# Optimization experiments

Hardware: AMD Instinct MI355X
Metric: run time of the kernel (lower is better)

## Reference

```python
import jax, jax.numpy as jnp
import numpy as np

B, H, S, D = 4, 16, 2048, 128


def setup_inputs() -> dict:
    key = jax.random.key(0)
    kq, kk, kv, km = jax.random.split(key, 4)
    query = jax.random.normal(kq, (B, H, S, D), dtype=jnp.float32)
    k = jax.random.normal(kk, (B, H, S, D), dtype=jnp.float32)
    value = jax.random.normal(kv, (B, H, S, D), dtype=jnp.float32)
    mask = jax.random.randint(km, (B, 1, S, S), 0, 2, dtype=jnp.int32)
    return {"query": query, "key": k, "value": value, "mask": mask, "softmax_dim": -1}


def reference(query, key, value, mask, softmax_dim):
    dk = query.shape[-1]
    # scores: [B, H, S, S]
    scores = jnp.einsum("bhqd,bhkd->bhqk", query, key) / jnp.sqrt(jnp.float32(dk))
    scores = jnp.where(mask == 0, jnp.float32(-1e9), scores)
    attention = jax.nn.softmax(scores, axis=softmax_dim)
    out = jnp.einsum("bhqk,bhkd->bhqd", attention, value)
    return (out, attention)
```

## Files before the change

kernel.cpp:

```cpp
#include <hip/hip_runtime.h>

typedef __attribute__((ext_vector_type(8))) short short8;
typedef __attribute__((ext_vector_type(4))) short short4v;
typedef __attribute__((ext_vector_type(4))) float float4v;

#define B_ 4
#define H_ 16
#define S_ 2048
#define D_ 128
#define BM 64
#define NKT64 32
#define NKT32 64

#define NSH (B_ * H_ * S_ * D_)
#define NMW ((size_t)B_ * 32 * S_)
#define WS_NEED (3ull * (unsigned long long)NSH * 2ull + (unsigned long long)NMW * 8ull)

#define QSCALE (0.08838834764831845f * 1.4426950408889634f)

__device__ __forceinline__ short f2bf(float f) {
  unsigned u = __float_as_uint(f);
  u = (u + 0x7fffu + ((u >> 16) & 1u)) >> 16;
  return (short)u;
}

__device__ __forceinline__ void gl16(const void* g, void* lds) {
  __builtin_amdgcn_global_load_lds(
      (const __attribute__((address_space(1))) unsigned int*)g,
      (__attribute__((address_space(3))) unsigned int*)lds, 16, 0, 0);
}

__global__ void prep_q(const float* __restrict__ Qg, short* __restrict__ Qb) {
  size_t id = (size_t)blockIdx.x * 256 + threadIdx.x;
  const float4v* src = (const float4v*)(Qg + id * 8);
  float4v a = src[0], b = src[1];
  short8 s;
  s[0] = f2bf(a[0] * QSCALE); s[1] = f2bf(a[1] * QSCALE);
  s[2] = f2bf(a[2] * QSCALE); s[3] = f2bf(a[3] * QSCALE);
  s[4] = f2bf(b[0] * QSCALE); s[5] = f2bf(b[1] * QSCALE);
  s[6] = f2bf(b[2] * QSCALE); s[7] = f2bf(b[3] * QSCALE);
  *((short8*)Qb + id) = s;
}

__global__ void prep_k(const float* __restrict__ Kg, short* __restrict__ Kf) {
  size_t id = (size_t)blockIdx.x * 256 + threadIdx.x;
  int c  = (int)(id & 15);
  int g  = (int)((id >> 4) & 3);
  int dc = (int)((id >> 6) & 3);
  int kf = (int)((id >> 8) & 3);
  int kt = (int)((id >> 10) & 31);
  size_t bh = id >> 15;
  const float* src = Kg + ((bh * S_ + (size_t)(kt * 64 + kf * 16 + c)) * D_) + dc * 32 + g * 8;
  float4v a = *(const float4v*)src;
  float4v b = *(const float4v*)(src + 4);
  short8 s;
  s[0] = f2bf(a[0]); s[1] = f2bf(a[1]); s[2] = f2bf(a[2]); s[3] = f2bf(a[3]);
  s[4] = f2bf(b[0]); s[5] = f2bf(b[1]); s[6] = f2bf(b[2]); s[7] = f2bf(b[3]);
  *((short8*)Kf + id) = s;
}

__global__ void prep_v(const float* __restrict__ Vg, short* __restrict__ Vf) {
  size_t id = (size_t)blockIdx.x * 256 + threadIdx.x;
  int c   = (int)(id & 15);
  int g   = (int)((id >> 4) & 3);
  int df  = (int)((id >> 6) & 7);
  int kt32= (int)((id >> 9) & 63);
  size_t bh = id >> 15;
  const float* src = Vg + (bh * S_ + (size_t)(kt32 * 32 + g * 8)) * D_ + df * 16 + c;
  short8 s;
#pragma unroll
  for (int e = 0; e < 8; ++e) s[e] = f2bf(src[(size_t)e * D_]);
  *((short8*)Vf + id) = s;
}

__global__ void prep_m(const int* __restrict__ Mg, unsigned long long* __restrict__ Bits) {
  int gw = blockIdx.x * 4 + (threadIdx.x >> 6);
  int j  = threadIdx.x & 63;
  int kt = gw & 31;
  int q  = (gw >> 5) & (S_ - 1);
  int b  = gw >> 16;
  int m = Mg[((size_t)b * S_ + q) * S_ + kt * 64 + j];
  unsigned long long bal = __ballot(m != 0);
  if (j == 0) Bits[((size_t)b * 32 + kt) * S_ + q] = bal;
}

__global__ __launch_bounds__(256, 4) void sdpa_main(
    const short* __restrict__ Qb, const short* __restrict__ Kfr,
    const short* __restrict__ Vfr, const unsigned long long* __restrict__ Bits,
    float* __restrict__ Og, float* __restrict__ Ag) {

  __shared__ __align__(16) char smem[32768 + 5120];
  short (*Ps)[40] = (short (*)[40])(smem + 32768);

  const int t = threadIdx.x;
  const int w = t >> 6;
  const int l = t & 63;
  const int g = l >> 4;
  const int c = l & 15;

  const int bid = blockIdx.x;
  const int qt = bid & 31;
  const int h  = (bid >> 5) & 15;
  const int b  = bid >> 9;

  const int qbase  = qt * BM;
  const int qrow_l = w * 16 + c;
  const int qrow   = qbase + qrow_l;

  const size_t bhOff = (size_t)(b * H_ + h) * (S_ * D_);
  const short* Qp  = Qb  + bhOff;
  const short* Kp  = Kfr + bhOff;
  const short* Vp  = Vfr + bhOff;
  const unsigned long long* Bp = Bits + (size_t)b * 32 * S_;
  const unsigned* Bu = (const unsigned*)Bits;
  float* Op = Og + bhOff;
  float* Ap = Ag + (size_t)(b * H_ + h) * ((size_t)S_ * S_);

  short8 qf[4];
#pragma unroll
  for (int dc = 0; dc < 4; ++dc)
    qf[dc] = *(const short8*)(Qp + (size_t)qrow * D_ + dc * 32 + g * 8);

#pragma unroll
  for (int i = 0; i < 4; ++i) {
    int f = w * 4 + i;
    gl16(Kp + f * 512 + l * 8, smem + f * 1024);
  }
  __syncthreads();

  float ls0 = 0.f, ls1 = 0.f, ls2 = 0.f, ls3 = 0.f;
  int cur = 0;
  for (int kt = 0; kt < NKT64; ++kt) {
    if (kt < NKT64 - 1) {
      const short* src = Kp + (size_t)(kt + 1) * 8192;
      char* dst = smem + (cur ^ 1) * 16384;
#pragma unroll
      for (int i = 0; i < 4; ++i) {
        int f = w * 4 + i;
        gl16(src + f * 512 + l * 8, dst + f * 1024);
      }
    }
    unsigned long long mb = Bp[(size_t)kt * S_ + qrow];
    const char* kb = smem + cur * 16384;

    float4v acc[4];
#pragma unroll
    for (int kf = 0; kf < 4; ++kf) acc[kf] = (float4v){0.f, 0.f, 0.f, 0.f};
#pragma unroll
    for (int kf = 0; kf < 4; ++kf) {
#pragma unroll
      for (int dc = 0; dc < 4; ++dc) {
        short8 af = *(const short8*)(kb + (kf * 4 + dc) * 1024 + l * 16);
        acc[kf] = __builtin_amdgcn_mfma_f32_16x16x32_bf16(af, qf[dc], acc[kf], 0, 0, 0);
      }
    }
#pragma unroll
    for (int kf = 0; kf < 4; ++kf) {
      unsigned mg = (unsigned)(mb >> (kf * 16 + g * 4)) & 0xFu;
      float p0 = ((mg >> 0) & 1) ? __builtin_amdgcn_exp2f(acc[kf][0]) : 0.f;
      float p1 = ((mg >> 1) & 1) ? __builtin_amdgcn_exp2f(acc[kf][1]) : 0.f;
      float p2 = ((mg >> 2) & 1) ? __builtin_amdgcn_exp2f(acc[kf][2]) : 0.f;
      float p3 = ((mg >> 3) & 1) ? __builtin_amdgcn_exp2f(acc[kf][3]) : 0.f;
      if (kf == 0) ls0 += (p0 + p1) + (p2 + p3);
      else if (kf == 1) ls1 += (p0 + p1) + (p2 + p3);
      else if (kf == 2) ls2 += (p0 + p1) + (p2 + p3);
      else ls3 += (p0 + p1) + (p2 + p3);
    }
    __syncthreads();
    cur ^= 1;
  }
  float lsum = (ls0 + ls1) + (ls2 + ls3);
  lsum += __shfl_xor(lsum, 16);
  lsum += __shfl_xor(lsum, 32);
  const float rl = (lsum > 0.f) ? (1.0f / lsum) : 0.f;

#pragma unroll
  for (int i = 0; i < 2; ++i) {
    int f = w + 4 * i;
    gl16(Kp + f * 512 + l * 8, smem + f * 1024);
    gl16(Vp + f * 512 + l * 8, smem + 16384 + f * 1024);
  }
  __syncthreads();

  float4v acco[8];
#pragma unroll
  for (int df = 0; df < 8; ++df) acco[df] = (float4v){0.f, 0.f, 0.f, 0.f};

  cur = 0;
  for (int kt = 0; kt < NKT32; ++kt) {
    if (kt < NKT32 - 1) {
      const short* ks = Kp + (size_t)(kt + 1) * 4096;
      const short* vs = Vp + (size_t)(kt + 1) * 4096;
      char* kd = smem + (cur ^ 1) * 8192;
      char* vd = smem + 16384 + (cur ^ 1) * 8192;
#pragma unroll
      for (int i = 0; i < 2; ++i) {
        int f = w + 4 * i;
        gl16(ks + f * 512 + l * 8, kd + f * 1024);
        gl16(vs + f * 512 + l * 8, vd + f * 1024);
      }
    }
    unsigned mw = Bu[((size_t)(b * 32 + (kt >> 1)) * S_ + qrow) * 2 + (kt & 1)];
    const char* kb = smem + cur * 8192;
    const char* vb = smem + 16384 + cur * 8192;

    float4v acc[2];
#pragma unroll
    for (int kf = 0; kf < 2; ++kf) acc[kf] = (float4v){0.f, 0.f, 0.f, 0.f};
#pragma unroll
    for (int kf = 0; kf < 2; ++kf) {
#pragma unroll
      for (int dc = 0; dc < 4; ++dc) {
        short8 af = *(const short8*)(kb + (kf * 4 + dc) * 1024 + l * 16);
        acc[kf] = __builtin_amdgcn_mfma_f32_16x16x32_bf16(af, qf[dc], acc[kf], 0, 0, 0);
      }
    }

#pragma unroll
    for (int kf = 0; kf < 2; ++kf) {
      int k0 = kt * 32 + kf * 16 + g * 4;
      unsigned mg = (mw >> (kf * 16 + g * 4)) & 0xFu;
      float4v aw;
      short4v pb;
#pragma unroll
      for (int r = 0; r < 4; ++r) {
        float pn = ((mg >> r) & 1) ? __builtin_amdgcn_exp2f(acc[kf][r]) * rl : 0.f;
        aw[r] = pn;
        pb[r] = f2bf(pn);
      }
      __builtin_nontemporal_store(aw, (float4v*)(Ap + (size_t)qrow * S_ + k0));
      *(short4v*)&Ps[qrow_l][kf * 16 + g * 4] = pb;
    }

    {
      short8 pbf = *(const short8*)&Ps[qrow_l][g * 8];
#pragma unroll
      for (int df = 0; df < 8; ++df) {
        short8 vf = *(const short8*)(vb + df * 1024 + l * 16);
        acco[df] = __builtin_amdgcn_mfma_f32_16x16x32_bf16(vf, pbf, acco[df], 0, 0, 0);
      }
    }
    __syncthreads();
    cur ^= 1;
  }

#pragma unroll
  for (int df = 0; df < 8; ++df) {
    *(float4v*)(Op + (size_t)qrow * D_ + df * 16 + g * 4) = acco[df];
  }
}

#define LQK 136
#define LVT 72

__global__ __launch_bounds__(256, 3) void sdpa_fallback(
    const float* __restrict__ Qg, const float* __restrict__ Kg,
    const float* __restrict__ Vg, const int* __restrict__ Mg,
    float* __restrict__ Og, float* __restrict__ Ag) {

  __shared__ __align__(16) char smemf[17408 + 27648];
  short (*Ks)[LQK]  = (short (*)[LQK])(smemf);
  short (*Qs)[LQK]  = (short (*)[LQK])(smemf + 17408);
  short (*VTs)[LVT] = (short (*)[LVT])(smemf + 17408);
  short (*Psf)[LVT] = (short (*)[LVT])(smemf + 17408 + 18432);

  const int t = threadIdx.x;
  const int w = t >> 6;
  const int l = t & 63;
  const int g = l >> 4;
  const int c = l & 15;

  const int bid = blockIdx.x;
  const int qt = bid & 31;
  const int h  = (bid >> 5) & 15;
  const int b  = bid >> 9;

  const int qbase  = qt * BM;
  const int qrow_l = w * 16 + c;
  const int qrow   = qbase + qrow_l;

  const size_t bhOff = (size_t)(b * H_ + h) * (S_ * D_);
  const float* Qp = Qg + bhOff;
  const float* Kp = Kg + bhOff;
  const float* Vp = Vg + bhOff;
  const int*   Mp = Mg + (size_t)b * S_ * S_;
  float* Op = Og + bhOff;
  float* Ap = Ag + (size_t)(b * H_ + h) * ((size_t)S_ * S_);

#pragma unroll
  for (int i = 0; i < 8; ++i) {
    int idx = t + i * 256;
    int d4 = idx & 31, row = idx >> 5;
    float4v v = *(const float4v*)(Qp + (size_t)(qbase + row) * D_ + d4 * 4);
    short4v s;
    s[0] = f2bf(v[0] * QSCALE); s[1] = f2bf(v[1] * QSCALE);
    s[2] = f2bf(v[2] * QSCALE); s[3] = f2bf(v[3] * QSCALE);
    *(short4v*)&Qs[row][d4 * 4] = s;
  }
  __syncthreads();

  short8 qf[4];
#pragma unroll
  for (int dc = 0; dc < 4; ++dc)
    qf[dc] = *(const short8*)&Qs[qrow_l][dc * 32 + g * 8];

  float m_run = -1e30f, l_run = 0.f;
  for (int kt = 0; kt < 32; ++kt) {
    __syncthreads();
#pragma unroll
    for (int i = 0; i < 8; ++i) {
      int idx = t + i * 256;
      int d4 = idx & 31, row = idx >> 5;
      float4v v = *(const float4v*)(Kp + (size_t)(kt * 64 + row) * D_ + d4 * 4);
      short4v s;
      s[0] = f2bf(v[0]); s[1] = f2bf(v[1]); s[2] = f2bf(v[2]); s[3] = f2bf(v[3]);
      *(short4v*)&Ks[row][d4 * 4] = s;
    }
    __syncthreads();

    float4v acc[4];
#pragma unroll
    for (int kf = 0; kf < 4; ++kf) acc[kf] = (float4v){0.f, 0.f, 0.f, 0.f};
#pragma unroll
    for (int kf = 0; kf < 4; ++kf) {
#pragma unroll
      for (int dc = 0; dc < 4; ++dc) {
        short8 af = *(const short8*)&Ks[kf * 16 + c][dc * 32 + g * 8];
        acc[kf] = __builtin_amdgcn_mfma_f32_16x16x32_bf16(af, qf[dc], acc[kf], 0, 0, 0);
      }
    }

    float sv[4][4];
    float tmax = -1e30f;
#pragma unroll
    for (int kf = 0; kf < 4; ++kf) {
      int k0 = kt * 64 + kf * 16 + g * 4;
      const int4 mv = *(const int4*)(Mp + (size_t)qrow * S_ + k0);
      int mr[4] = {mv.x, mv.y, mv.z, mv.w};
#pragma unroll
      for (int r = 0; r < 4; ++r) {
        float x = acc[kf][r];
        x = (mr[r] == 0) ? -1e9f : x;
        sv[kf][r] = x;
        tmax = fmaxf(tmax, x);
      }
    }
    tmax = fmaxf(tmax, __shfl_xor(tmax, 16));
    tmax = fmaxf(tmax, __shfl_xor(tmax, 32));
    float newm = fmaxf(m_run, tmax);
    float tsum = 0.f;
#pragma unroll
    for (int kf = 0; kf < 4; ++kf)
#pragma unroll
      for (int r = 0; r < 4; ++r)
        tsum += __builtin_amdgcn_exp2f(sv[kf][r] - newm);
    tsum += __shfl_xor(tsum, 16);
    tsum += __shfl_xor(tsum, 32);
    l_run = l_run * __builtin_amdgcn_exp2f(m_run - newm) + tsum;
    m_run = newm;
  }

  const float rl = 1.0f / l_run;

  float4v acco[8];
#pragma unroll
  for (int df = 0; df < 8; ++df) acco[df] = (float4v){0.f, 0.f, 0.f, 0.f};

  for (int kt = 0; kt < 32; ++kt) {
    __syncthreads();
#pragma unroll
    for (int i = 0; i < 8; ++i) {
      int idx = t + i * 256;
      int d4 = idx & 31, row = idx >> 5;
      float4v v = *(const float4v*)(Kp + (size_t)(kt * 64 + row) * D_ + d4 * 4);
      short4v s;
      s[0] = f2bf(v[0]); s[1] = f2bf(v[1]); s[2] = f2bf(v[2]); s[3] = f2bf(v[3]);
      *(short4v*)&Ks[row][d4 * 4] = s;
    }
#pragma unroll
    for (int i = 0; i < 8; ++i) {
      int idx = t + i * 256;
      int d = idx & 127, kq = idx >> 7;
      const float* vp = Vp + (size_t)(kt * 64 + kq * 4) * D_ + d;
      short4v s;
      s[0] = f2bf(vp[0]); s[1] = f2bf(vp[D_]); s[2] = f2bf(vp[2 * D_]); s[3] = f2bf(vp[3 * D_]);
      *(short4v*)&VTs[d][kq * 4] = s;
    }
    __syncthreads();

    float4v acc[4];
#pragma unroll
    for (int kf = 0; kf < 4; ++kf) acc[kf] = (float4v){0.f, 0.f, 0.f, 0.f};
#pragma unroll
    for (int kf = 0; kf < 4; ++kf) {
#pragma unroll
      for (int dc = 0; dc < 4; ++dc) {
        short8 af = *(const short8*)&Ks[kf * 16 + c][dc * 32 + g * 8];
        acc[kf] = __builtin_amdgcn_mfma_f32_16x16x32_bf16(af, qf[dc], acc[kf], 0, 0, 0);
      }
    }

#pragma unroll
    for (int kf = 0; kf < 4; ++kf) {
      int k0 = kt * 64 + kf * 16 + g * 4;
      const int4 mv = *(const int4*)(Mp + (size_t)qrow * S_ + k0);
      int mr[4] = {mv.x, mv.y, mv.z, mv.w};
      float4v aw;
      short4v pb;
#pragma unroll
      for (int r = 0; r < 4; ++r) {
        float x = acc[kf][r];
        x = (mr[r] == 0) ? -1e9f : x;
        float pn = __builtin_amdgcn_exp2f(x - m_run) * rl;
        aw[r] = pn;
        pb[r] = f2bf(pn);
      }
      __builtin_nontemporal_store(aw, (float4v*)(Ap + (size_t)qrow * S_ + k0));
      *(short4v*)&Psf[qrow_l][kf * 16 + g * 4] = pb;
    }

#pragma unroll
    for (int kc = 0; kc < 2; ++kc) {
      short8 pbf = *(const short8*)&Psf[qrow_l][kc * 32 + g * 8];
#pragma unroll
      for (int df = 0; df < 8; ++df) {
        short8 vf = *(const short8*)&VTs[df * 16 + c][kc * 32 + g * 8];
        acco[df] = __builtin_amdgcn_mfma_f32_16x16x32_bf16(vf, pbf, acco[df], 0, 0, 0);
      }
    }
  }

#pragma unroll
  for (int df = 0; df < 8; ++df) {
    *(float4v*)(Op + (size_t)qrow * D_ + df * 16 + g * 4) = acco[df];
  }
}

extern "C" void kernel_launch(void* const* d_in, const int* in_sizes, int n_in,
                              void* d_out, int out_size, void* d_ws, size_t ws_size,
                              hipStream_t stream) {
  const float* Q = (const float*)d_in[0];
  const float* K = (const float*)d_in[1];
  const float* V = (const float*)d_in[2];
  const int*   M = (const int*)d_in[3];
  float* Out  = (float*)d_out;
  float* Attn = Out + (size_t)B_ * H_ * S_ * D_;

  if (ws_size >= WS_NEED) {
    short* Qb = (short*)d_ws;
    short* Kf = Qb + (size_t)NSH;
    short* Vf = Kf + (size_t)NSH;
    unsigned long long* Bits = (unsigned long long*)(Vf + (size_t)NSH);
    const int pgrid = NSH / 8 / 256;
    prep_q<<<dim3(pgrid), dim3(256), 0, stream>>>(Q, Qb);
    prep_k<<<dim3(pgrid), dim3(256), 0, stream>>>(K, Kf);
    prep_v<<<dim3(pgrid), dim3(256), 0, stream>>>(V, Vf);
    prep_m<<<dim3((unsigned)(NMW / 4)), dim3(256), 0, stream>>>(M, Bits);
    sdpa_main<<<dim3(B_ * H_ * (S_ / BM)), dim3(256), 0, stream>>>(Qb, Kf, Vf, Bits, Out, Attn);
  } else {
    sdpa_fallback<<<dim3(B_ * H_ * (S_ / BM)), dim3(256), 0, stream>>>(Q, K, V, M, Out, Attn);
  }
}
```

Measured before the change: 456.9 us.

## Split row-sum pass into separate kernel, use hardware bf16 pack and priority hints

The first pass that computes softmax denominators moves out of the main kernel into its own kernel. It uses 32-key tiles, smaller LDS and a higher occupancy bound, and writes log2 of each row sum to the workspace. The main kernel folds normalization into the exp2 argument by subtracting the log-sum, prefetches the next mask word, and raises wave priority around the MFMA blocks. Software bf16 rounding is replaced with the v_cvt_pk_bf16_f32 instruction in both the prep kernels and the P packing, and the output stores become nontemporal. This costs an extra kernel launch and a small workspace buffer, and QK^T is still computed twice.

```diff
diff --git a/kernel.cpp b/kernel.cpp
--- a/kernel.cpp
+++ b/kernel.cpp
@@ -9,14 +9,20 @@
 #define S_ 2048
 #define D_ 128
 #define BM 64
-#define NKT64 32
 #define NKT32 64
 
 #define NSH (B_ * H_ * S_ * D_)
 #define NMW ((size_t)B_ * 32 * S_)
-#define WS_NEED (3ull * (unsigned long long)NSH * 2ull + (unsigned long long)NMW * 8ull)
+#define NLG ((size_t)B_ * H_ * S_)
+#define WS_NEED (3ull * (unsigned long long)NSH * 2ull + (unsigned long long)NMW * 8ull + (unsigned long long)NLG * 4ull)
 
 #define QSCALE (0.08838834764831845f * 1.4426950408889634f)
+
+__device__ __forceinline__ unsigned cvtpk(float lo, float hi) {
+  unsigned r;
+  asm("v_cvt_pk_bf16_f32 %0, %1, %2" : "=v"(r) : "v"(lo), "v"(hi));
+  return r;
+}
 
 __device__ __forceinline__ short f2bf(float f) {
   unsigned u = __float_as_uint(f);
@@ -34,12 +40,12 @@
   size_t id = (size_t)blockIdx.x * 256 + threadIdx.x;
   const float4v* src = (const float4v*)(Qg + id * 8);
   float4v a = src[0], b = src[1];
-  short8 s;
-  s[0] = f2bf(a[0] * QSCALE); s[1] = f2bf(a[1] * QSCALE);
-  s[2] = f2bf(a[2] * QSCALE); s[3] = f2bf(a[3] * QSCALE);
-  s[4] = f2bf(b[0] * QSCALE); s[5] = f2bf(b[1] * QSCALE);
-  s[6] = f2bf(b[2] * QSCALE); s[7] = f2bf(b[3] * QSCALE);
-  *((short8*)Qb + id) = s;
+  int4 s;
+  s.x = (int)cvtpk(a[0] * QSCALE, a[1] * QSCALE);
+  s.y = (int)cvtpk(a[2] * QSCALE, a[3] * QSCALE);
+  s.z = (int)cvtpk(b[0] * QSCALE, b[1] * QSCALE);
+  s.w = (int)cvtpk(b[2] * QSCALE, b[3] * QSCALE);
+  ((int4*)Qb)[id] = s;
 }
 
 __global__ void prep_k(const float* __restrict__ Kg, short* __restrict__ Kf) {
@@ -53,10 +59,12 @@
   const float* src = Kg + ((bh * S_ + (size_t)(kt * 64 + kf * 16 + c)) * D_) + dc * 32 + g * 8;
   float4v a = *(const float4v*)src;
   float4v b = *(const float4v*)(src + 4);
-  short8 s;
-  s[0] = f2bf(a[0]); s[1] = f2bf(a[1]); s[2] = f2bf(a[2]); s[3] = f2bf(a[3]);
-  s[4] = f2bf(b[0]); s[5] = f2bf(b[1]); s[6] = f2bf(b[2]); s[7] = f2bf(b[3]);
-  *((short8*)Kf + id) = s;
+  int4 s;
+  s.x = (int)cvtpk(a[0], a[1]);
+  s.y = (int)cvtpk(a[2], a[3]);
+  s.z = (int)cvtpk(b[0], b[1]);
+  s.w = (int)cvtpk(b[2], b[3]);
+  ((int4*)Kf)[id] = s;
 }
 
 __global__ void prep_v(const float* __restrict__ Vg, short* __restrict__ Vf) {
@@ -67,10 +75,15 @@
   int kt32= (int)((id >> 9) & 63);
   size_t bh = id >> 15;
   const float* src = Vg + (bh * S_ + (size_t)(kt32 * 32 + g * 8)) * D_ + df * 16 + c;
-  short8 s;
-#pragma unroll
-  for (int e = 0; e < 8; ++e) s[e] = f2bf(src[(size_t)e * D_]);
-  *((short8*)Vf + id) = s;
+  float f[8];
+#pragma unroll
+  for (int e = 0; e < 8; ++e) f[e] = src[(size_t)e * D_];
+  int4 s;
+  s.x = (int)cvtpk(f[0], f[1]);
+  s.y = (int)cvtpk(f[2], f[3]);
+  s.z = (int)cvtpk(f[4], f[5]);
+  s.w = (int)cvtpk(f[6], f[7]);
+  ((int4*)Vf)[id] = s;
 }
 
 __global__ void prep_m(const int* __restrict__ Mg, unsigned long long* __restrict__ Bits) {
@@ -84,37 +97,28 @@
   if (j == 0) Bits[((size_t)b * 32 + kt) * S_ + q] = bal;
 }
 
-__global__ __launch_bounds__(256, 4) void sdpa_main(
+__global__ __launch_bounds__(256, 8) void sums_kernel(
     const short* __restrict__ Qb, const short* __restrict__ Kfr,
-    const short* __restrict__ Vfr, const unsigned long long* __restrict__ Bits,
-    float* __restrict__ Og, float* __restrict__ Ag) {
-
-  __shared__ __align__(16) char smem[32768 + 5120];
-  short (*Ps)[40] = (short (*)[40])(smem + 32768);
+    const unsigned* __restrict__ Bu, float* __restrict__ Lg) {
+
+  __shared__ __align__(16) char smem[16384];
 
   const int t = threadIdx.x;
   const int w = t >> 6;
   const int l = t & 63;
   const int g = l >> 4;
-  const int c = l & 15;
 
   const int bid = blockIdx.x;
   const int qt = bid & 31;
   const int h  = (bid >> 5) & 15;
   const int b  = bid >> 9;
 
-  const int qbase  = qt * BM;
-  const int qrow_l = w * 16 + c;
-  const int qrow   = qbase + qrow_l;
+  const int qbase = qt * BM;
+  const int qrow  = qbase + w * 16 + (l & 15);
 
   const size_t bhOff = (size_t)(b * H_ + h) * (S_ * D_);
-  const short* Qp  = Qb  + bhOff;
-  const short* Kp  = Kfr + bhOff;
-  const short* Vp  = Vfr + bhOff;
-  const unsigned long long* Bp = Bits + (size_t)b * 32 * S_;
-  const unsigned* Bu = (const unsigned*)Bits;
-  float* Op = Og + bhOff;
-  float* Ap = Ag + (size_t)(b * H_ + h) * ((size_t)S_ * S_);
+  const short* Qp = Qb  + bhOff;
+  const short* Kp = Kfr + bhOff;
 
   short8 qf[4];
 #pragma unroll
@@ -122,57 +126,97 @@
     qf[dc] = *(const short8*)(Qp + (size_t)qrow * D_ + dc * 32 + g * 8);
 
 #pragma unroll
-  for (int i = 0; i < 4; ++i) {
-    int f = w * 4 + i;
+  for (int i = 0; i < 2; ++i) {
+    int f = w + 4 * i;
     gl16(Kp + f * 512 + l * 8, smem + f * 1024);
   }
   __syncthreads();
 
-  float ls0 = 0.f, ls1 = 0.f, ls2 = 0.f, ls3 = 0.f;
+  float ls0 = 0.f, ls1 = 0.f;
   int cur = 0;
-  for (int kt = 0; kt < NKT64; ++kt) {
-    if (kt < NKT64 - 1) {
-      const short* src = Kp + (size_t)(kt + 1) * 8192;
-      char* dst = smem + (cur ^ 1) * 16384;
-#pragma unroll
-      for (int i = 0; i < 4; ++i) {
-        int f = w * 4 + i;
-        gl16(src + f * 512 + l * 8, dst + f * 1024);
-      }
-    }
-    unsigned long long mb = Bp[(size_t)kt * S_ + qrow];
-    const char* kb = smem + cur * 16384;
-
-    float4v acc[4];
-#pragma unroll
-    for (int kf = 0; kf < 4; ++kf) acc[kf] = (float4v){0.f, 0.f, 0.f, 0.f};
-#pragma unroll
-    for (int kf = 0; kf < 4; ++kf) {
+  for (int kt = 0; kt < NKT32; ++kt) {
+    if (kt < NKT32 - 1) {
+      const short* ks = Kp + (size_t)(kt + 1) * 4096;
+      char* kd = smem + (cur ^ 1) * 8192;
+#pragma unroll
+      for (int i = 0; i < 2; ++i) {
+        int f = w + 4 * i;
+        gl16(ks + f * 512 + l * 8, kd + f * 1024);
+      }
+    }
+    unsigned mw = Bu[((size_t)(b * 32 + (kt >> 1)) * S_ + qrow) * 2 + (kt & 1)];
+    const char* kb = smem + cur * 8192;
+
+    float4v acc[2];
+#pragma unroll
+    for (int kf = 0; kf < 2; ++kf) acc[kf] = (float4v){0.f, 0.f, 0.f, 0.f};
+    __builtin_amdgcn_s_setprio(1);
+#pragma unroll
+    for (int kf = 0; kf < 2; ++kf) {
 #pragma unroll
       for (int dc = 0; dc < 4; ++dc) {
         short8 af = *(const short8*)(kb + (kf * 4 + dc) * 1024 + l * 16);
         acc[kf] = __builtin_amdgcn_mfma_f32_16x16x32_bf16(af, qf[dc], acc[kf], 0, 0, 0);
       }
     }
-#pragma unroll
-    for (int kf = 0; kf < 4; ++kf) {
-      unsigned mg = (unsigned)(mb >> (kf * 16 + g * 4)) & 0xFu;
+    __builtin_amdgcn_s_setprio(0);
+#pragma unroll
+    for (int kf = 0; kf < 2; ++kf) {
+      unsigned mg = (mw >> (kf * 16 + g * 4)) & 0xFu;
       float p0 = ((mg >> 0) & 1) ? __builtin_amdgcn_exp2f(acc[kf][0]) : 0.f;
       float p1 = ((mg >> 1) & 1) ? __builtin_amdgcn_exp2f(acc[kf][1]) : 0.f;
       float p2 = ((mg >> 2) & 1) ? __builtin_amdgcn_exp2f(acc[kf][2]) : 0.f;
       float p3 = ((mg >> 3) & 1) ? __builtin_amdgcn_exp2f(acc[kf][3]) : 0.f;
       if (kf == 0) ls0 += (p0 + p1) + (p2 + p3);
-      else if (kf == 1) ls1 += (p0 + p1) + (p2 + p3);
-      else if (kf == 2) ls2 += (p0 + p1) + (p2 + p3);
-      else ls3 += (p0 + p1) + (p2 + p3);
+      else         ls1 += (p0 + p1) + (p2 + p3);
     }
     __syncthreads();
     cur ^= 1;
   }
-  float lsum = (ls0 + ls1) + (ls2 + ls3);
+  float lsum = ls0 + ls1;
   lsum += __shfl_xor(lsum, 16);
   lsum += __shfl_xor(lsum, 32);
-  const float rl = (lsum > 0.f) ? (1.0f / lsum) : 0.f;
+  if (l < 16)
+    Lg[(size_t)(b * H_ + h) * S_ + qbase + w * 16 + l] =
+        (lsum > 0.f) ? __log2f(lsum) : 1e30f;
+}
+
+__global__ __launch_bounds__(256, 4) void sdpa_main(
+    const short* __restrict__ Qb, const short* __restrict__ Kfr,
+    const short* __restrict__ Vfr, const unsigned* __restrict__ Bu,
+    const float* __restrict__ Lg,
+    float* __restrict__ Og, float* __restrict__ Ag) {
+
+  __shared__ __align__(16) char smem[32768 + 5120];
+  short (*Ps)[40] = (short (*)[40])(smem + 32768);
+
+  const int t = threadIdx.x;
+  const int w = t >> 6;
+  const int l = t & 63;
+  const int g = l >> 4;
+
+  const int bid = blockIdx.x;
+  const int qt = bid & 31;
+  const int h  = (bid >> 5) & 15;
+  const int b  = bid >> 9;
+
+  const int qbase  = qt * BM;
+  const int qrow_l = w * 16 + (l & 15);
+  const int qrow   = qbase + qrow_l;
+
+  const size_t bhOff = (size_t)(b * H_ + h) * (S_ * D_);
+  const short* Qp = Qb  + bhOff;
+  const short* Kp = Kfr + bhOff;
+  const short* Vp = Vfr + bhOff;
+  float* Op = Og + bhOff;
+  float* Ap = Ag + (size_t)(b * H_ + h) * ((size_t)S_ * S_);
+
+  const float lg = Lg[(size_t)(b * H_ + h) * S_ + qrow];
+
+  short8 qf[4];
+#pragma unroll
+  for (int dc = 0; dc < 4; ++dc)
+    qf[dc] = *(const short8*)(Qp + (size_t)qrow * D_ + dc * 32 + g * 8);
 
 #pragma unroll
   for (int i = 0; i < 2; ++i) {
@@ -186,9 +230,12 @@
 #pragma unroll
   for (int df = 0; df < 8; ++df) acco[df] = (float4v){0.f, 0.f, 0.f, 0.f};
 
-  cur = 0;
+  unsigned mw = Bu[((size_t)(b * 32) * S_ + qrow) * 2];
+  int cur = 0;
   for (int kt = 0; kt < NKT32; ++kt) {
+    unsigned mw_next = 0;
     if (kt < NKT32 - 1) {
+      mw_next = Bu[((size_t)(b * 32 + ((kt + 1) >> 1)) * S_ + qrow) * 2 + ((kt + 1) & 1)];
       const short* ks = Kp + (size_t)(kt + 1) * 4096;
       const short* vs = Vp + (size_t)(kt + 1) * 4096;
       char* kd = smem + (cur ^ 1) * 8192;
@@ -200,13 +247,13 @@
         gl16(vs + f * 512 + l * 8, vd + f * 1024);
       }
     }
-    unsigned mw = Bu[((size_t)(b * 32 + (kt >> 1)) * S_ + qrow) * 2 + (kt & 1)];
     const char* kb = smem + cur * 8192;
     const char* vb = smem + 16384 + cur * 8192;
 
     float4v acc[2];
 #pragma unroll
     for (int kf = 0; kf < 2; ++kf) acc[kf] = (float4v){0.f, 0.f, 0.f, 0.f};
+    __builtin_amdgcn_s_setprio(1);
 #pragma unroll
     for (int kf = 0; kf < 2; ++kf) {
 #pragma unroll
@@ -215,38 +262,43 @@
         acc[kf] = __builtin_amdgcn_mfma_f32_16x16x32_bf16(af, qf[dc], acc[kf], 0, 0, 0);
       }
     }
+    __builtin_amdgcn_s_setprio(0);
 
 #pragma unroll
     for (int kf = 0; kf < 2; ++kf) {
       int k0 = kt * 32 + kf * 16 + g * 4;
       unsigned mg = (mw >> (kf * 16 + g * 4)) & 0xFu;
       float4v aw;
-      short4v pb;
 #pragma unroll
       for (int r = 0; r < 4; ++r) {
-        float pn = ((mg >> r) & 1) ? __builtin_amdgcn_exp2f(acc[kf][r]) * rl : 0.f;
-        aw[r] = pn;
-        pb[r] = f2bf(pn);
-      }
+        float arg = ((mg >> r) & 1) ? (acc[kf][r] - lg) : -1e30f;
+        aw[r] = __builtin_amdgcn_exp2f(arg);
+      }
+      int2 pb;
+      pb.x = (int)cvtpk(aw[0], aw[1]);
+      pb.y = (int)cvtpk(aw[2], aw[3]);
       __builtin_nontemporal_store(aw, (float4v*)(Ap + (size_t)qrow * S_ + k0));
-      *(short4v*)&Ps[qrow_l][kf * 16 + g * 4] = pb;
+      *(int2*)&Ps[qrow_l][kf * 16 + g * 4] = pb;
     }
 
     {
       short8 pbf = *(const short8*)&Ps[qrow_l][g * 8];
+      __builtin_amdgcn_s_setprio(1);
 #pragma unroll
       for (int df = 0; df < 8; ++df) {
         short8 vf = *(const short8*)(vb + df * 1024 + l * 16);
         acco[df] = __builtin_amdgcn_mfma_f32_16x16x32_bf16(vf, pbf, acco[df], 0, 0, 0);
       }
+      __builtin_amdgcn_s_setprio(0);
     }
     __syncthreads();
+    mw = mw_next;
     cur ^= 1;
   }
 
 #pragma unroll
   for (int df = 0; df < 8; ++df) {
-    *(float4v*)(Op + (size_t)qrow * D_ + df * 16 + g * 4) = acco[df];
+    __builtin_nontemporal_store(acco[df], (float4v*)(Op + (size_t)qrow * D_ + df * 16 + g * 4));
   }
 }
 
@@ -451,12 +503,16 @@
     short* Kf = Qb + (size_t)NSH;
     short* Vf = Kf + (size_t)NSH;
     unsigned long long* Bits = (unsigned long long*)(Vf + (size_t)NSH);
+    float* Lg = (float*)(Bits + NMW);
     const int pgrid = NSH / 8 / 256;
     prep_q<<<dim3(pgrid), dim3(256), 0, stream>>>(Q, Qb);
     prep_k<<<dim3(pgrid), dim3(256), 0, stream>>>(K, Kf);
+    prep_m<<<dim3((unsigned)(NMW / 4)), dim3(256), 0, stream>>>(M, Bits);
     prep_v<<<dim3(pgrid), dim3(256), 0, stream>>>(V, Vf);
-    prep_m<<<dim3((unsigned)(NMW / 4)), dim3(256), 0, stream>>>(M, Bits);
-    sdpa_main<<<dim3(B_ * H_ * (S_ / BM)), dim3(256), 0, stream>>>(Qb, Kf, Vf, Bits, Out, Attn);
+    sums_kernel<<<dim3(B_ * H_ * (S_ / BM)), dim3(256), 0, stream>>>(
+        Qb, Kf, (const unsigned*)Bits, Lg);
+    sdpa_main<<<dim3(B_ * H_ * (S_ / BM)), dim3(256), 0, stream>>>(
+        Qb, Kf, Vf, (const unsigned*)Bits, Lg, Out, Attn);
   } else {
     sdpa_fallback<<<dim3(B_ * H_ * (S_ / BM)), dim3(256), 0, stream>>>(Q, K, V, M, Out, Attn);
   }
```

After: 508.6 us. 11.3% more time.
